# Kernel optimization log

Measured on AMD Instinct MI355X. Metric: run time of the kernel, lower is better.

The kernel has to match this reference:

```python
import jax, jax.numpy as jnp
import numpy as np

N_NODES = 100000
N_EDGES = 1600000
IN_C, HID_C, OUT_C = 128, 128, 64


def setup_inputs() -> dict:
    key = jax.random.key(0)
    ks = jax.random.split(key, 6)
    x = jax.random.normal(ks[0], (N_NODES, IN_C), dtype=jnp.float32)
    edge_index = jax.random.randint(ks[1], (2, N_EDGES), 0, N_NODES)
    W1 = jax.random.normal(ks[2], (IN_C, HID_C), dtype=jnp.float32) * (1.0 / np.sqrt(IN_C))
    b1 = jnp.zeros((HID_C,), dtype=jnp.float32)
    W2 = jax.random.normal(ks[3], (HID_C, OUT_C), dtype=jnp.float32) * (1.0 / np.sqrt(HID_C))
    b2 = jnp.zeros((OUT_C,), dtype=jnp.float32)
    return {"x": x, "edge_index": edge_index, "W1": W1, "b1": b1, "W2": W2, "b2": b2}


def gcn_conv(x, W, b, src, dst):
    # PyG GCNConv: D^{-1/2} (A + I) D^{-1/2} X W + b, with self-loops handled
    # analytically (no explicit self-loop edges materialized).
    h = x @ W                                             # [N, d_out]
    ones = jnp.ones(src.shape[0], dtype=h.dtype)
    deg = jax.ops.segment_sum(ones, dst, num_segments=N_NODES) + 1.0  # +1 self-loop
    dinv = jax.lax.rsqrt(deg)                             # deg >= 1, safe
    norm = dinv[src] * dinv[dst]                          # [E]
    msg = h[src] * norm[:, None]                          # gather + scale  [E, d_out]
    agg = jax.ops.segment_sum(msg, dst, num_segments=N_NODES)
    agg = agg + h * (dinv * dinv)[:, None]                # self-loop contribution
    return agg + b


def reference(x, edge_index, W1, b1, W2, b2):
    src, dst = edge_index[0], edge_index[1]
    h = jax.nn.relu(gcn_conv(x, W1, b1, src, dst))
    # dropout is identity in eval mode
    out = gcn_conv(h, W2, b2, src, dst)
    return out
```

## Files before the change

kernel.cpp:

```cpp
#include <hip/hip_runtime.h>

#define N_NODESC 100000
#define N_EDGESC 1600000
#define NB_BUCKETS 391
#define BUCKET_CAP 5120
#define CHUNK_A 4096

typedef __attribute__((ext_vector_type(4))) float floatx4;
typedef __attribute__((ext_vector_type(8))) short shortx8;

__device__ __forceinline__ unsigned short f32_to_bf16_rne(float f) {
    unsigned int u = __float_as_uint(f);
    unsigned int r = u + 0x7fffu + ((u >> 16) & 1u);
    return (unsigned short)(r >> 16);
}
__device__ __forceinline__ float bf16_to_f32(unsigned short h) {
    return __uint_as_float(((unsigned int)h) << 16);
}
__device__ __forceinline__ float bflo(unsigned int u) { return __uint_as_float(u << 16); }
__device__ __forceinline__ float bfhi(unsigned int u) { return __uint_as_float(u & 0xffff0000u); }
__device__ __forceinline__ unsigned int pack2bf(float a, float b) {
    return ((unsigned int)f32_to_bf16_rne(b) << 16) | (unsigned int)f32_to_bf16_rne(a);
}

__global__ __launch_bounds__(256) void k_wfrag_all(const float* __restrict__ W1,
        const float* __restrict__ W2,
        unsigned short* __restrict__ w1hi, unsigned short* __restrict__ w1lo,
        unsigned short* __restrict__ w2hi, unsigned short* __restrict__ w2lo,
        int* __restrict__ gcur) {
    int t = threadIdx.x;
    if (blockIdx.x == 0)
        for (int i = t; i < NB_BUCKETS; i += 256) gcur[i] = i * BUCKET_CAP;
    int idx = blockIdx.x * 256 + t;
    float f;
    int k, col, C, o;
    unsigned short *phi, *plo;
    if (idx < 16384) {
        k = idx >> 7; col = idx & 127; C = 8;
        f = W1[idx]; phi = w1hi; plo = w1lo;
    } else {
        int idx2 = idx - 16384;
        k = idx2 >> 6; col = idx2 & 63; C = 4;
        f = W2[idx2]; phi = w2hi; plo = w2lo;
    }
    unsigned short hi = f32_to_bf16_rne(f);
    unsigned short lo = f32_to_bf16_rne(f - bf16_to_f32(hi));
    int kc = k >> 5, q = (k >> 3) & 3, j = k & 7;
    int c = col >> 4, n = col & 15;
    o = (((kc * C + c) * 4 + q) * 16 + n) * 8 + j;
    phi[o] = hi; plo[o] = lo;
}

__global__ __launch_bounds__(1024) void k_bucket(const int* __restrict__ src,
        const int* __restrict__ dst, int* __restrict__ gcur,
        unsigned int* __restrict__ tmp) {
    __shared__ int hist[NB_BUCKETS];
    int t = threadIdx.x;
    for (int i = t; i < NB_BUCKETS; i += 1024) hist[i] = 0;
    __syncthreads();
    int base = blockIdx.x * CHUNK_A;
    int end = min(base + CHUNK_A, N_EDGESC);
    unsigned int cv[4];
    int cb[4];
#pragma unroll
    for (int k = 0; k < 4; ++k) {
        int e = base + t + k * 1024;
        cb[k] = -1;
        if (e < end) {
            int s = src[e], d = dst[e];
            cv[k] = ((unsigned int)s << 8) | (unsigned int)(d & 255);
            cb[k] = d >> 8;
            atomicAdd(&hist[cb[k]], 1);
        }
    }
    __syncthreads();
    for (int i = t; i < NB_BUCKETS; i += 1024) {
        int c = hist[i];
        hist[i] = (c > 0) ? atomicAdd(&gcur[i], c) : 0;
    }
    __syncthreads();
#pragma unroll
    for (int k = 0; k < 4; ++k) {
        if (cb[k] >= 0) {
            int pos = atomicAdd(&hist[cb[k]], 1);
            tmp[pos] = cv[k];
        }
    }
}

__global__ __launch_bounds__(1024) void k_place(const unsigned int* __restrict__ tmp,
        const int* __restrict__ gcur,
        int* __restrict__ swsrc, int* __restrict__ deg,
        int* __restrict__ row_ptr, float* __restrict__ dinv) {
    __shared__ unsigned int eb[BUCKET_CAP];
    __shared__ int hist[256], scan[256], lcur[256];
    int b = blockIdx.x, t = threadIdx.x;
    int start = b * BUCKET_CAP;
    int cnt = gcur[b] - start;
    if (t < 256) hist[t] = 0;
    for (int i = t; i < cnt; i += 1024) eb[i] = tmp[start + i];
    __syncthreads();
    for (int i = t; i < cnt; i += 1024)
        atomicAdd(&hist[eb[i] & 255u], 1);
    __syncthreads();
    int own = (t < 256) ? hist[t] : 0;
    if (t < 256) scan[t] = own;
    __syncthreads();
    for (int off = 1; off < 256; off <<= 1) {
        int add = (t >= off && t < 256) ? scan[t - off] : 0;
        __syncthreads();
        if (t < 256) scan[t] += add;
        __syncthreads();
    }
    if (t < 256) {
        int rp = start + scan[t] - own;
        lcur[t] = rp;
        int node = (b << 8) + t;
        if (node < N_NODESC) {
            deg[node] = own;
            row_ptr[node] = rp;
            dinv[node] = rsqrtf((float)own + 1.0f);
        }
    }
    __syncthreads();
    for (int i = t; i < cnt; i += 1024) {
        unsigned int v = eb[i];
        int pos = atomicAdd(&lcur[v & 255u], 1);
        swsrc[pos] = (int)(v >> 8);
    }
}

template<int NOUT, int AFP32>
__global__ __launch_bounds__(256) void k_gemm_mfma(const void* __restrict__ Xv,
        const unsigned short* __restrict__ whi, const unsigned short* __restrict__ wlo,
        const float* __restrict__ dinv, unsigned short* __restrict__ H) {
    constexpr int C = NOUT / 16;
    constexpr int PITCH = NOUT + 4;
    __shared__ __align__(16) float etile[4][16][PITCH];
    int wv = threadIdx.x >> 6, lane = threadIdx.x & 63;
    int n16 = lane & 15, q = lane >> 4;
    int rowBase = blockIdx.x * 128 + wv * 32;
    floatx4 acc[2][C];
#pragma unroll
    for (int m = 0; m < 2; ++m)
#pragma unroll
        for (int c = 0; c < C; ++c) acc[m][c] = (floatx4){0.f, 0.f, 0.f, 0.f};

    const shortx8* whi8 = (const shortx8*)whi;
    const shortx8* wlo8 = (const shortx8*)wlo;

    for (int kc = 0; kc < 4; ++kc) {
        shortx8 ahi[2], alo[2];
#pragma unroll
        for (int m = 0; m < 2; ++m) {
            int r = rowBase + m * 16 + n16;
            if (r >= N_NODESC) r = N_NODESC - 1;
            if (AFP32) {
                const float* xp = &((const float*)Xv)[(size_t)r * 128 + kc * 32 + q * 8];
                floatx4 x0 = *(const floatx4*)xp;
                floatx4 x1 = *(const floatx4*)(xp + 4);
#pragma unroll
                for (int jj = 0; jj < 4; ++jj) {
                    unsigned short h0 = f32_to_bf16_rne(x0[jj]);
                    ahi[m][jj] = (short)h0;
                    alo[m][jj] = (short)f32_to_bf16_rne(x0[jj] - bf16_to_f32(h0));
                    unsigned short h1 = f32_to_bf16_rne(x1[jj]);
                    ahi[m][jj + 4] = (short)h1;
                    alo[m][jj + 4] = (short)f32_to_bf16_rne(x1[jj] - bf16_to_f32(h1));
                }
            } else {
                const unsigned short* xp = &((const unsigned short*)Xv)[(size_t)r * 128 + kc * 32 + q * 8];
                ahi[m] = *(const shortx8*)xp;
            }
        }
#pragma unroll
        for (int c = 0; c < C; ++c) {
            int fo = (kc * C + c) * 64 + lane;
            shortx8 bhi = whi8[fo];
            shortx8 blo = wlo8[fo];
#pragma unroll
            for (int m = 0; m < 2; ++m) {
                acc[m][c] = __builtin_amdgcn_mfma_f32_16x16x32_bf16(ahi[m], bhi, acc[m][c], 0, 0, 0);
                if (AFP32)
                    acc[m][c] = __builtin_amdgcn_mfma_f32_16x16x32_bf16(alo[m], bhi, acc[m][c], 0, 0, 0);
                acc[m][c] = __builtin_amdgcn_mfma_f32_16x16x32_bf16(ahi[m], blo, acc[m][c], 0, 0, 0);
            }
        }
    }
    constexpr int CPL = NOUT / 4;
#pragma unroll
    for (int m = 0; m < 2; ++m) {
        __builtin_amdgcn_wave_barrier();
#pragma unroll
        for (int c = 0; c < C; ++c)
#pragma unroll
            for (int reg = 0; reg < 4; ++reg)
                etile[wv][q * 4 + reg][c * 16 + n16] = acc[m][c][reg];
        asm volatile("s_waitcnt lgkmcnt(0)" ::: "memory");
        __builtin_amdgcn_wave_barrier();
        int row = lane >> 2, cb = lane & 3;
        int r = rowBase + m * 16 + row;
        if (r < N_NODESC) {
            float dv = dinv[r];
            unsigned int po[CPL / 2];
#pragma unroll
            for (int i = 0; i < CPL / 4; ++i) {
                floatx4 v = *(const floatx4*)&etile[wv][row][cb * CPL + i * 4];
                po[i * 2 + 0] = pack2bf(v[0] * dv, v[1] * dv);
                po[i * 2 + 1] = pack2bf(v[2] * dv, v[3] * dv);
            }
            unsigned int* op = (unsigned int*)&H[(size_t)r * NOUT + cb * CPL];
#pragma unroll
            for (int i = 0; i < CPL / 8; ++i)
                *(uint4*)(op + i * 4) = *(uint4*)&po[i * 4];
        }
        asm volatile("s_waitcnt lgkmcnt(0)" ::: "memory");
        __builtin_amdgcn_wave_barrier();
    }
}

__global__ __launch_bounds__(256) void k_agg_gemm(const unsigned short* __restrict__ Hb,
        const int* __restrict__ swsrc, const int* __restrict__ row_ptr,
        const int* __restrict__ deg, const float* __restrict__ dinv,
        const float* __restrict__ bias,
        const unsigned short* __restrict__ w2hi, const unsigned short* __restrict__ w2lo,
        unsigned short* __restrict__ H2) {
    __shared__ __align__(16) unsigned int lds_h[16][64];
    int wv = threadIdx.x >> 6, lane = threadIdx.x & 63;
    int g = lane >> 4, l16 = lane & 15;
    int nb = blockIdx.x * 16;

#pragma unroll
    for (int i = 0; i < 4; ++i) {
        int nt = wv * 4 + i;
        int node = nb + nt;
        int start = row_ptr[node];
        int end = start + deg[node];
        float acc[8] = {0.f, 0.f, 0.f, 0.f, 0.f, 0.f, 0.f, 0.f};
        int j = start + g;
        for (; j + 4 < end; j += 8) {
            int s0 = swsrc[j];
            int s1 = swsrc[j + 4];
            uint4 v0 = *(const uint4*)(Hb + (size_t)s0 * 128 + l16 * 8);
            uint4 v1 = *(const uint4*)(Hb + (size_t)s1 * 128 + l16 * 8);
            acc[0] += bflo(v0.x) + bflo(v1.x);
            acc[1] += bfhi(v0.x) + bfhi(v1.x);
            acc[2] += bflo(v0.y) + bflo(v1.y);
            acc[3] += bfhi(v0.y) + bfhi(v1.y);
            acc[4] += bflo(v0.z) + bflo(v1.z);
            acc[5] += bfhi(v0.z) + bfhi(v1.z);
            acc[6] += bflo(v0.w) + bflo(v1.w);
            acc[7] += bfhi(v0.w) + bfhi(v1.w);
        }
        if (j < end) {
            int s0 = swsrc[j];
            uint4 v0 = *(const uint4*)(Hb + (size_t)s0 * 128 + l16 * 8);
            acc[0] += bflo(v0.x); acc[1] += bfhi(v0.x);
            acc[2] += bflo(v0.y); acc[3] += bfhi(v0.y);
            acc[4] += bflo(v0.z); acc[5] += bfhi(v0.z);
            acc[6] += bflo(v0.w); acc[7] += bfhi(v0.w);
        }
#pragma unroll
        for (int k = 0; k < 8; ++k) {
            acc[k] += __shfl_xor(acc[k], 16);
            acc[k] += __shfl_xor(acc[k], 32);
        }
        if (g == 0) {
            float dv = dinv[node];
            uint4 sv = *(const uint4*)(Hb + (size_t)node * 128 + l16 * 8);
            floatx4 b0 = *(const floatx4*)&bias[l16 * 8];
            floatx4 b1 = *(const floatx4*)&bias[l16 * 8 + 4];
            float o0 = dv * (acc[0] + bflo(sv.x)) + b0[0];
            float o1 = dv * (acc[1] + bfhi(sv.x)) + b0[1];
            float o2 = dv * (acc[2] + bflo(sv.y)) + b0[2];
            float o3 = dv * (acc[3] + bfhi(sv.y)) + b0[3];
            float o4 = dv * (acc[4] + bflo(sv.z)) + b1[0];
            float o5 = dv * (acc[5] + bfhi(sv.z)) + b1[1];
            float o6 = dv * (acc[6] + bflo(sv.w)) + b1[2];
            float o7 = dv * (acc[7] + bfhi(sv.w)) + b1[3];
            uint4 o;
            o.x = pack2bf(fmaxf(o0, 0.f), fmaxf(o1, 0.f));
            o.y = pack2bf(fmaxf(o2, 0.f), fmaxf(o3, 0.f));
            o.z = pack2bf(fmaxf(o4, 0.f), fmaxf(o5, 0.f));
            o.w = pack2bf(fmaxf(o6, 0.f), fmaxf(o7, 0.f));
            int pcol = (l16 * 4) ^ ((nt & 7) * 4);
            *(uint4*)&lds_h[nt][pcol] = o;
        }
    }
    __syncthreads();

    int q = lane >> 4, n16 = lane & 15;
    floatx4 accm = (floatx4){0.f, 0.f, 0.f, 0.f};
    const shortx8* whi8 = (const shortx8*)w2hi;
    const shortx8* wlo8 = (const shortx8*)w2lo;
#pragma unroll
    for (int kc = 0; kc < 4; ++kc) {
        int pcol = (kc * 16 + q * 4) ^ ((n16 & 7) * 4);
        shortx8 ahi = *(const shortx8*)&lds_h[n16][pcol];
        int fo = (kc * 4 + wv) * 64 + lane;
        shortx8 bhi = whi8[fo];
        shortx8 blo = wlo8[fo];
        accm = __builtin_amdgcn_mfma_f32_16x16x32_bf16(ahi, bhi, accm, 0, 0, 0);
        accm = __builtin_amdgcn_mfma_f32_16x16x32_bf16(ahi, blo, accm, 0, 0, 0);
    }
    int crow = (lane >> 4) * 4;
    int ccol = wv * 16 + n16;
#pragma unroll
    for (int reg = 0; reg < 4; ++reg) {
        int r = nb + crow + reg;
        float dv = dinv[r];
        H2[(size_t)r * 64 + ccol] = f32_to_bf16_rne(accm[reg] * dv);
    }
}

__global__ __launch_bounds__(256) void k_agg64(const unsigned short* __restrict__ Hb,
        const int* __restrict__ swsrc, const int* __restrict__ row_ptr,
        const int* __restrict__ deg, const float* __restrict__ dinv,
        const float* __restrict__ bias, float* __restrict__ out) {
    int node = blockIdx.x * 4 + (threadIdx.x >> 6);
    int lane = threadIdx.x & 63;
    int g = lane >> 3, l8 = lane & 7;
    int start = row_ptr[node];
    int end = start + deg[node];
    float acc[8] = {0.f, 0.f, 0.f, 0.f, 0.f, 0.f, 0.f, 0.f};
    int j = start + g;
    for (; j + 8 < end; j += 16) {
        int s0 = swsrc[j];
        int s1 = swsrc[j + 8];
        uint4 v0 = *(const uint4*)(Hb + (size_t)s0 * 64 + l8 * 8);
        uint4 v1 = *(const uint4*)(Hb + (size_t)s1 * 64 + l8 * 8);
        acc[0] += bflo(v0.x) + bflo(v1.x);
        acc[1] += bfhi(v0.x) + bfhi(v1.x);
        acc[2] += bflo(v0.y) + bflo(v1.y);
        acc[3] += bfhi(v0.y) + bfhi(v1.y);
        acc[4] += bflo(v0.z) + bflo(v1.z);
        acc[5] += bfhi(v0.z) + bfhi(v1.z);
        acc[6] += bflo(v0.w) + bflo(v1.w);
        acc[7] += bfhi(v0.w) + bfhi(v1.w);
    }
    if (j < end) {
        int s0 = swsrc[j];
        uint4 v0 = *(const uint4*)(Hb + (size_t)s0 * 64 + l8 * 8);
        acc[0] += bflo(v0.x); acc[1] += bfhi(v0.x);
        acc[2] += bflo(v0.y); acc[3] += bfhi(v0.y);
        acc[4] += bflo(v0.z); acc[5] += bfhi(v0.z);
        acc[6] += bflo(v0.w); acc[7] += bfhi(v0.w);
    }
#pragma unroll
    for (int i = 0; i < 8; ++i) {
        acc[i] += __shfl_xor(acc[i], 8);
        acc[i] += __shfl_xor(acc[i], 16);
        acc[i] += __shfl_xor(acc[i], 32);
    }
    if (g == 0) {
        float dv = dinv[node];
        uint4 sv = *(const uint4*)(Hb + (size_t)node * 64 + l8 * 8);
        floatx4 b0 = *(const floatx4*)&bias[l8 * 8];
        floatx4 b1 = *(const floatx4*)&bias[l8 * 8 + 4];
        floatx4 o0, o1;
        o0[0] = dv * (acc[0] + bflo(sv.x)) + b0[0];
        o0[1] = dv * (acc[1] + bfhi(sv.x)) + b0[1];
        o0[2] = dv * (acc[2] + bflo(sv.y)) + b0[2];
        o0[3] = dv * (acc[3] + bfhi(sv.y)) + b0[3];
        o1[0] = dv * (acc[4] + bflo(sv.z)) + b1[0];
        o1[1] = dv * (acc[5] + bfhi(sv.z)) + b1[1];
        o1[2] = dv * (acc[6] + bflo(sv.w)) + b1[2];
        o1[3] = dv * (acc[7] + bfhi(sv.w)) + b1[3];
        *(floatx4*)&out[(size_t)node * 64 + l8 * 8] = o0;
        *(floatx4*)&out[(size_t)node * 64 + l8 * 8 + 4] = o1;
    }
}

extern "C" void kernel_launch(void* const* d_in, const int* in_sizes, int n_in,
                              void* d_out, int out_size, void* d_ws, size_t ws_size,
                              hipStream_t stream) {
    const float* x  = (const float*)d_in[0];
    const int*   ei = (const int*)d_in[1];
    const float* W1 = (const float*)d_in[2];
    const float* b1 = (const float*)d_in[3];
    const float* W2 = (const float*)d_in[4];
    const float* b2 = (const float*)d_in[5];
    float* out = (float*)d_out;
    const int* src = ei;
    const int* dst = ei + N_EDGESC;

    char* ws = (char*)d_ws;
    size_t off = 0;
    auto alloc = [&](size_t bytes) -> void* {
        off = (off + 255) & ~(size_t)255;
        void* p = ws + off;
        off += bytes;
        return p;
    };
    const size_t CSR_SLOTS = (size_t)NB_BUCKETS * BUCKET_CAP;
    int*   deg     = (int*)  alloc((size_t)N_NODESC * 4);
    float* dinv    = (float*)alloc((size_t)N_NODESC * 4);
    int*   row_ptr = (int*)  alloc((size_t)N_NODESC * 4);
    int*   gcur    = (int*)  alloc(NB_BUCKETS * 4);
    unsigned int* tmp   = (unsigned int*)alloc(CSR_SLOTS * 4);
    int*   swsrc   = (int*)  alloc(CSR_SLOTS * 4);
    unsigned short* w1hi = (unsigned short*)alloc(128 * 128 * 2);
    unsigned short* w1lo = (unsigned short*)alloc(128 * 128 * 2);
    unsigned short* w2hi = (unsigned short*)alloc(128 * 64 * 2);
    unsigned short* w2lo = (unsigned short*)alloc(128 * 64 * 2);
    unsigned short* h1b  = (unsigned short*)alloc((size_t)N_NODESC * 128 * 2);
    unsigned short* h2b  = (unsigned short*)alloc((size_t)N_NODESC * 128 * 2);

    const int nbGemm = (N_NODESC + 127) / 128;
    const int nbBkt  = (N_EDGESC + CHUNK_A - 1) / CHUNK_A;

    k_wfrag_all<<<(16384 + 8192) / 256, 256, 0, stream>>>(W1, W2, w1hi, w1lo, w2hi, w2lo, gcur);
    k_bucket<<<nbBkt, 1024, 0, stream>>>(src, dst, gcur, tmp);
    k_place<<<NB_BUCKETS, 1024, 0, stream>>>(tmp, gcur, swsrc, deg, row_ptr, dinv);

    k_gemm_mfma<128, 1><<<nbGemm, 256, 0, stream>>>(x, w1hi, w1lo, dinv, h1b);
    k_agg_gemm<<<N_NODESC / 16, 256, 0, stream>>>(h1b, swsrc, row_ptr, deg, dinv, b1,
                                                  w2hi, w2lo, h2b);
    k_agg64<<<N_NODESC / 4, 256, 0, stream>>>(h2b, swsrc, row_ptr, deg, dinv, b2, out);
}
```

Baseline: 275.8 us.

## Split CSR placement per half-bucket and dynamically schedule nodes in aggregation

k_place now runs two blocks per bucket, each handling 128 of the 256 destination nodes. The upper half derives its row offsets from the bucket end, which doubles parallelism at the cost of each block reading the full bucket. k_agg_gemm processes 32 nodes with 8 waves per block, where waves grab nodes from an LDS atomic counter to balance uneven degrees. The MFMA stage is remapped to 2 row groups by 4 column groups.

```diff
diff --git a/kernel.cpp b/kernel.cpp
--- a/kernel.cpp
+++ b/kernel.cpp
@@ -93,29 +93,35 @@
         int* __restrict__ swsrc, int* __restrict__ deg,
         int* __restrict__ row_ptr, float* __restrict__ dinv) {
     __shared__ unsigned int eb[BUCKET_CAP];
-    __shared__ int hist[256], scan[256], lcur[256];
-    int b = blockIdx.x, t = threadIdx.x;
+    __shared__ int hist[128], scan[128], lcur[128];
+    int b2 = blockIdx.x, t = threadIdx.x;
+    int b = b2 >> 1, h = b2 & 1;
     int start = b * BUCKET_CAP;
-    int cnt = gcur[b] - start;
-    if (t < 256) hist[t] = 0;
+    int end = gcur[b];
+    int cnt = end - start;
+    if (t < 128) hist[t] = 0;
     for (int i = t; i < cnt; i += 1024) eb[i] = tmp[start + i];
     __syncthreads();
-    for (int i = t; i < cnt; i += 1024)
-        atomicAdd(&hist[eb[i] & 255u], 1);
-    __syncthreads();
-    int own = (t < 256) ? hist[t] : 0;
-    if (t < 256) scan[t] = own;
-    __syncthreads();
-    for (int off = 1; off < 256; off <<= 1) {
-        int add = (t >= off && t < 256) ? scan[t - off] : 0;
+    for (int i = t; i < cnt; i += 1024) {
+        unsigned int v = eb[i];
+        if ((int)((v >> 7) & 1u) == h) atomicAdd(&hist[v & 127u], 1);
+    }
+    __syncthreads();
+    int own = (t < 128) ? hist[t] : 0;
+    if (t < 128) scan[t] = own;
+    __syncthreads();
+    for (int off = 1; off < 128; off <<= 1) {
+        int add = (t >= off && t < 128) ? scan[t - off] : 0;
         __syncthreads();
-        if (t < 256) scan[t] += add;
+        if (t < 128) scan[t] += add;
         __syncthreads();
     }
-    if (t < 256) {
-        int rp = start + scan[t] - own;
+    int total = scan[127];
+    if (t < 128) {
+        int excl = scan[t] - own;
+        int rp = h ? (end - total + excl) : (start + excl);
         lcur[t] = rp;
-        int node = (b << 8) + t;
+        int node = (b << 8) + (h << 7) + t;
         if (node < N_NODESC) {
             deg[node] = own;
             row_ptr[node] = rp;
@@ -125,8 +131,10 @@
     __syncthreads();
     for (int i = t; i < cnt; i += 1024) {
         unsigned int v = eb[i];
-        int pos = atomicAdd(&lcur[v & 255u], 1);
-        swsrc[pos] = (int)(v >> 8);
+        if ((int)((v >> 7) & 1u) == h) {
+            int pos = atomicAdd(&lcur[v & 127u], 1);
+            swsrc[pos] = (int)(v >> 8);
+        }
     }
 }
 
@@ -219,21 +227,26 @@
     }
 }
 
-__global__ __launch_bounds__(256) void k_agg_gemm(const unsigned short* __restrict__ Hb,
+__global__ __launch_bounds__(512) void k_agg_gemm(const unsigned short* __restrict__ Hb,
         const int* __restrict__ swsrc, const int* __restrict__ row_ptr,
         const int* __restrict__ deg, const float* __restrict__ dinv,
         const float* __restrict__ bias,
         const unsigned short* __restrict__ w2hi, const unsigned short* __restrict__ w2lo,
         unsigned short* __restrict__ H2) {
-    __shared__ __align__(16) unsigned int lds_h[16][64];
+    __shared__ __align__(16) unsigned int lds_h[32][64];
+    __shared__ int nxt;
     int wv = threadIdx.x >> 6, lane = threadIdx.x & 63;
     int g = lane >> 4, l16 = lane & 15;
-    int nb = blockIdx.x * 16;
-
-#pragma unroll
-    for (int i = 0; i < 4; ++i) {
-        int nt = wv * 4 + i;
-        int node = nb + nt;
+    int nb = blockIdx.x * 32;
+    if (threadIdx.x == 0) nxt = 0;
+    __syncthreads();
+
+    for (;;) {
+        int n;
+        if (lane == 0) n = atomicAdd(&nxt, 1);
+        n = __shfl(n, 0);
+        if (n >= 32) break;
+        int node = nb + n;
         int start = row_ptr[node];
         int end = start + deg[node];
         float acc[8] = {0.f, 0.f, 0.f, 0.f, 0.f, 0.f, 0.f, 0.f};
@@ -283,31 +296,32 @@
             o.y = pack2bf(fmaxf(o2, 0.f), fmaxf(o3, 0.f));
             o.z = pack2bf(fmaxf(o4, 0.f), fmaxf(o5, 0.f));
             o.w = pack2bf(fmaxf(o6, 0.f), fmaxf(o7, 0.f));
-            int pcol = (l16 * 4) ^ ((nt & 7) * 4);
-            *(uint4*)&lds_h[nt][pcol] = o;
+            int pcol = (l16 * 4) ^ ((n & 7) * 4);
+            *(uint4*)&lds_h[n][pcol] = o;
         }
     }
     __syncthreads();
 
     int q = lane >> 4, n16 = lane & 15;
+    int rowgrp = wv >> 2, colgrp = wv & 3;
     floatx4 accm = (floatx4){0.f, 0.f, 0.f, 0.f};
     const shortx8* whi8 = (const shortx8*)w2hi;
     const shortx8* wlo8 = (const shortx8*)w2lo;
 #pragma unroll
     for (int kc = 0; kc < 4; ++kc) {
         int pcol = (kc * 16 + q * 4) ^ ((n16 & 7) * 4);
-        shortx8 ahi = *(const shortx8*)&lds_h[n16][pcol];
-        int fo = (kc * 4 + wv) * 64 + lane;
+        shortx8 ahi = *(const shortx8*)&lds_h[rowgrp * 16 + n16][pcol];
+        int fo = (kc * 4 + colgrp) * 64 + lane;
         shortx8 bhi = whi8[fo];
         shortx8 blo = wlo8[fo];
         accm = __builtin_amdgcn_mfma_f32_16x16x32_bf16(ahi, bhi, accm, 0, 0, 0);
         accm = __builtin_amdgcn_mfma_f32_16x16x32_bf16(ahi, blo, accm, 0, 0, 0);
     }
-    int crow = (lane >> 4) * 4;
-    int ccol = wv * 16 + n16;
+    int crow = q * 4;
+    int ccol = colgrp * 16 + n16;
 #pragma unroll
     for (int reg = 0; reg < 4; ++reg) {
-        int r = nb + crow + reg;
+        int r = nb + rowgrp * 16 + crow + reg;
         float dv = dinv[r];
         H2[(size_t)r * 64 + ccol] = f32_to_bf16_rne(accm[reg] * dv);
     }
@@ -411,10 +425,10 @@
 
     k_wfrag_all<<<(16384 + 8192) / 256, 256, 0, stream>>>(W1, W2, w1hi, w1lo, w2hi, w2lo, gcur);
     k_bucket<<<nbBkt, 1024, 0, stream>>>(src, dst, gcur, tmp);
-    k_place<<<NB_BUCKETS, 1024, 0, stream>>>(tmp, gcur, swsrc, deg, row_ptr, dinv);
+    k_place<<<NB_BUCKETS * 2, 1024, 0, stream>>>(tmp, gcur, swsrc, deg, row_ptr, dinv);
 
     k_gemm_mfma<128, 1><<<nbGemm, 256, 0, stream>>>(x, w1hi, w1lo, dinv, h1b);
-    k_agg_gemm<<<N_NODESC / 16, 256, 0, stream>>>(h1b, swsrc, row_ptr, deg, dinv, b1,
+    k_agg_gemm<<<N_NODESC / 32, 512, 0, stream>>>(h1b, swsrc, row_ptr, deg, dinv, b1,
                                                   w2hi, w2lo, h2b);
     k_agg64<<<N_NODESC / 4, 256, 0, stream>>>(h2b, swsrc, row_ptr, deg, dinv, b2, out);
 }
```

Measured after the change: 281.0 us. Within noise of the previous version (+1.9%).
